# Optimization experiments

Hardware: AMD Instinct MI355X
Metric: run time of the kernel (lower is better)

## Reference

```python
import jax, jax.numpy as jnp
import numpy as np

H = 512

def setup_inputs() -> dict:
    key = jax.random.key(0)
    ks = jax.random.split(key, 8)
    b, s, m, n, h = 8, 128, 32, 64, H
    sc = 1.0 / np.sqrt(h)
    return {
        "x": jax.random.normal(ks[0], (b, s, m, h), dtype=jnp.float32),
        "y": jax.random.normal(ks[1], (b, s, n, h), dtype=jnp.float32),
        # MultiHeadSelfAtt (additive self-attentive pooling: b*m*h -> b*h)
        "Wa1": jax.random.normal(ks[2], (h, h), dtype=jnp.float32) * sc,
        "ba1": jnp.zeros((h,), dtype=jnp.float32),
        "wa2": jax.random.normal(ks[3], (h,), dtype=jnp.float32) * sc,
        # gate Linear(2h -> h), torch layout weight: (h, 2h)
        "Wl": jax.random.normal(ks[4], (h, 2 * h), dtype=jnp.float32) * (1.0 / np.sqrt(2 * h)),
        "bl": jnp.zeros((h,), dtype=jnp.float32),
    }

def reference(x, y, Wa1, ba1, wa2, Wl, bl):
    h = x.shape[-1]
    # attentive pooling over m for every (b, s) slice: b s m h -> b s h
    scores = jnp.tanh(x @ Wa1 + ba1) @ wa2          # b s m
    attn = jax.nn.softmax(scores, axis=-1)
    pooled = jnp.einsum('bsm,bsmh->bsh', attn, x)   # b s h
    # step i (i>=1) uses pooled x at step i-1
    i_x = pooled[:, :-1]                            # b (s-1) h
    Wy, Wi = Wl[:, :h], Wl[:, h:]                   # split concat-linear
    pre = jnp.einsum('bsnh,gh->bsng', y[:, 1:], Wy) \
        + (i_x @ Wi.T + bl)[:, :, None, :]          # b (s-1) n h
    gate = jax.nn.sigmoid(pre)
    out_rest = y[:, 1:] + i_x[:, :, None, :] * gate
    return jnp.concatenate([y[:, :1], out_rest], axis=1)  # b s n h
```

## Files before the change

### kernel.cpp

```cpp
#include <hip/hip_runtime.h>
#include <cstdint>
#include <cstddef>

#define H 512
#define SEQ 128

typedef __bf16 v8bf __attribute__((ext_vector_type(8)));
typedef float v4f __attribute__((ext_vector_type(4)));

__device__ __forceinline__ unsigned short f2bf(float f) {
    unsigned int u = __float_as_uint(f);
    u = (u + 0x7FFFu + ((u >> 16) & 1u)) >> 16;
    return (unsigned short)u;
}
__device__ __forceinline__ float bf2f(unsigned short h) {
    return __uint_as_float(((unsigned int)h) << 16);
}
__device__ __forceinline__ v8bf load_bf8(const unsigned short* p) {
    return *reinterpret_cast<const v8bf*>(p);
}
__device__ __forceinline__ float fast_tanh(float v) {
    float e = __expf(2.f * v);
    return 1.f - 2.f * __builtin_amdgcn_rcpf(e + 1.f);
}
__device__ __forceinline__ float fast_sigmoid(float v) {
    return __builtin_amdgcn_rcpf(1.f + __expf(-v));
}


__global__ __launch_bounds__(256) void prep_kernel(
        const float* __restrict__ Wa1, const float* __restrict__ Wl,
        unsigned short* __restrict__ WyS, unsigned short* __restrict__ WiS,
        unsigned short* __restrict__ WaS) {
    int tg = blockIdx.x * 256 + threadIdx.x;
    int mat = tg >> 15;
    int idx = tg & 32767;
    int lane = idx & 63;
    int ks = (idx >> 6) & 15;
    int c = idx >> 10;
    int g = c * 16 + (lane & 15);
    int hb = ks * 32 + ((lane >> 4) << 3);
    unsigned short o[8];
    unsigned short* dst;
    if (mat == 0) {
        const float* s = Wl + (size_t)g * 1024 + hb;
#pragma unroll
        for (int j = 0; j < 8; ++j) o[j] = f2bf(s[j]);
        dst = WyS + (size_t)idx * 8;
    } else if (mat == 1) {
        const float* s = Wl + (size_t)g * 1024 + 512 + hb;
#pragma unroll
        for (int j = 0; j < 8; ++j) o[j] = f2bf(s[j]);
        dst = WiS + (size_t)idx * 8;
    } else {
#pragma unroll
        for (int j = 0; j < 8; ++j) o[j] = f2bf(Wa1[(size_t)(hb + j) * H + g]);
        dst = WaS + (size_t)idx * 8;
    }
    *reinterpret_cast<ushort4*>(dst)     = *reinterpret_cast<ushort4*>(&o[0]);
    *reinterpret_cast<ushort4*>(dst + 4) = *reinterpret_cast<ushort4*>(&o[4]);
}

__global__ __launch_bounds__(256, 3) void attn_pool_kernel(
        const float* __restrict__ x, const unsigned short* __restrict__ WaS,
        const float* __restrict__ ba1, const float* __restrict__ wa2,
        float* __restrict__ ixf, unsigned short* __restrict__ ixb) {
    __shared__ __align__(16) unsigned short Xb[32][520];
    __shared__ float attn[32];
    __shared__ float scpart[4][32];

    int bid = blockIdx.x;
    int b = bid / 127, s = bid % 127;
    int t = threadIdx.x;

    const float4* x4 = reinterpret_cast<const float4*>(x + (size_t)(b * SEQ + s) * 32 * H);
#pragma unroll
    for (int i = 0; i < 16; ++i) {
        int idx4 = t + i * 256;
        float4 v = x4[idx4];
        int e = idx4 * 4, m = e >> 9, h = e & 511;
        ushort4 o;
        o.x = f2bf(v.x); o.y = f2bf(v.y); o.z = f2bf(v.z); o.w = f2bf(v.w);
        *reinterpret_cast<ushort4*>(&Xb[m][h]) = o;
    }
    __syncthreads();

    int w = t >> 6, lane = t & 63, q = lane >> 4, c16 = lane & 15;

    v4f acc[2][8];
#pragma unroll
    for (int mi = 0; mi < 2; ++mi)
#pragma unroll
        for (int ci = 0; ci < 8; ++ci) acc[mi][ci] = (v4f){0.f, 0.f, 0.f, 0.f};

    const unsigned short* Bb = WaS + (size_t)(w * 8 * 16) * 512 + lane * 8;

#pragma unroll
    for (int ks = 0; ks < 16; ++ks) {
        v8bf a0 = load_bf8(&Xb[c16][ks * 32 + q * 8]);
        v8bf a1 = load_bf8(&Xb[16 + c16][ks * 32 + q * 8]);
#pragma unroll
        for (int ci = 0; ci < 8; ++ci) {
            v8bf bb = load_bf8(Bb + (size_t)(ci * 16 + ks) * 512);
            acc[0][ci] = __builtin_amdgcn_mfma_f32_16x16x32_bf16(a0, bb, acc[0][ci], 0, 0, 0);
            acc[1][ci] = __builtin_amdgcn_mfma_f32_16x16x32_bf16(a1, bb, acc[1][ci], 0, 0, 0);
        }
    }

    float sr[2][4] = {{0.f, 0.f, 0.f, 0.f}, {0.f, 0.f, 0.f, 0.f}};
#pragma unroll
    for (int ci = 0; ci < 8; ++ci) {
        int g = (w * 8 + ci) * 16 + c16;
        float w2 = wa2[g];
        float bv = ba1[g];
#pragma unroll
        for (int mi = 0; mi < 2; ++mi)
#pragma unroll
            for (int i = 0; i < 4; ++i)
                sr[mi][i] += w2 * fast_tanh(acc[mi][ci][i] + bv);
    }
#pragma unroll
    for (int off = 1; off < 16; off <<= 1) {
#pragma unroll
        for (int mi = 0; mi < 2; ++mi)
#pragma unroll
            for (int i = 0; i < 4; ++i) sr[mi][i] += __shfl_xor(sr[mi][i], off);
    }
    if (c16 == 0) {
#pragma unroll
        for (int mi = 0; mi < 2; ++mi)
#pragma unroll
            for (int i = 0; i < 4; ++i) scpart[w][mi * 16 + q * 4 + i] = sr[mi][i];
    }
    __syncthreads();

    if (t == 0) {
        float sc[32];
        float mx = -1e30f;
#pragma unroll
        for (int m = 0; m < 32; ++m) {
            float v = scpart[0][m] + scpart[1][m] + scpart[2][m] + scpart[3][m];
            sc[m] = v;
            mx = fmaxf(mx, v);
        }
        float sum = 0.f;
#pragma unroll
        for (int m = 0; m < 32; ++m) {
            float e = __expf(sc[m] - mx);
            attn[m] = e;
            sum += e;
        }
        float inv = 1.f / sum;
#pragma unroll
        for (int m = 0; m < 32; ++m) attn[m] *= inv;
    }
    __syncthreads();

    int h0 = t * 2;
    float p0 = 0.f, p1 = 0.f;
#pragma unroll
    for (int m = 0; m < 32; ++m) {
        float am = attn[m];
        p0 += am * bf2f(Xb[m][h0]);
        p1 += am * bf2f(Xb[m][h0 + 1]);
    }
    size_t r = (size_t)bid;
    ixf[r * H + h0] = p0;
    ixf[r * H + h0 + 1] = p1;
    ixb[r * H + h0] = f2bf(p0);
    ixb[r * H + h0 + 1] = f2bf(p1);
}

__global__ __launch_bounds__(256) void ipre_kernel(
        const unsigned short* __restrict__ ixb, const unsigned short* __restrict__ WiS,
        const float* __restrict__ bl, float* __restrict__ ipre) {
    int row16 = blockIdx.x * 16;
    int t = threadIdx.x, w = t >> 6, lane = t & 63, q = lane >> 4, c16 = lane & 15;
    int c0 = blockIdx.y * 8 + w * 2;

    v4f acc0 = {0.f, 0.f, 0.f, 0.f};
    v4f acc1 = {0.f, 0.f, 0.f, 0.f};
    const unsigned short* arow = ixb + (size_t)(row16 + c16) * H + q * 8;
#pragma unroll
    for (int ks = 0; ks < 16; ++ks) {
        v8bf a = load_bf8(arow + ks * 32);
        acc0 = __builtin_amdgcn_mfma_f32_16x16x32_bf16(
            a, load_bf8(WiS + (size_t)(c0 * 16 + ks) * 512 + lane * 8), acc0, 0, 0, 0);
        acc1 = __builtin_amdgcn_mfma_f32_16x16x32_bf16(
            a, load_bf8(WiS + (size_t)((c0 + 1) * 16 + ks) * 512 + lane * 8), acc1, 0, 0, 0);
    }
#pragma unroll
    for (int cc = 0; cc < 2; ++cc) {
        int g = (c0 + cc) * 16 + c16;
        float blv = bl[g];
        v4f a = cc ? acc1 : acc0;
#pragma unroll
        for (int i = 0; i < 4; ++i) {
            int row = row16 + q * 4 + i;
            if (row < 1016) ipre[(size_t)row * H + g] = a[i] + blv;
        }
    }
}

__global__ __launch_bounds__(256, 2) void main_kernel(
        const float* __restrict__ y, const unsigned short* __restrict__ WyS,
        const float* __restrict__ ixf, const float* __restrict__ ipre,
        float* __restrict__ out) {
    int s = blockIdx.x, b = blockIdx.y;
    int t = threadIdx.x;
    size_t base = (size_t)(b * SEQ + s) * 64 * H;

    if (s == 0) {
        const float4* y4 = reinterpret_cast<const float4*>(y + base);
        float4* o4 = reinterpret_cast<float4*>(out + base);
#pragma unroll
        for (int i = 0; i < 32; ++i) o4[t + i * 256] = y4[t + i * 256];
        return;
    }

    __shared__ __align__(16) unsigned short Yb[64][520];
    __shared__ float ip_s[512];
    __shared__ float ix_s[512];

    int r = b * 127 + (s - 1);
    const float4* y4 = reinterpret_cast<const float4*>(y + base);
#pragma unroll
    for (int i = 0; i < 32; ++i) {
        int idx4 = t + i * 256;
        float4 v = y4[idx4];
        int e = idx4 * 4, n = e >> 9, h = e & 511;
        ushort4 o;
        o.x = f2bf(v.x); o.y = f2bf(v.y); o.z = f2bf(v.z); o.w = f2bf(v.w);
        *reinterpret_cast<ushort4*>(&Yb[n][h]) = o;
    }
    ip_s[t]       = ipre[(size_t)r * H + t];
    ip_s[t + 256] = ipre[(size_t)r * H + t + 256];
    ix_s[t]       = ixf[(size_t)r * H + t];
    ix_s[t + 256] = ixf[(size_t)r * H + t + 256];
    __syncthreads();

    int w = t >> 6, lane = t & 63, q = lane >> 4, c16 = lane & 15;

#pragma unroll
    for (int pass = 0; pass < 2; ++pass) {
        v4f acc[4][4];
#pragma unroll
        for (int rt = 0; rt < 4; ++rt)
#pragma unroll
            for (int ci = 0; ci < 4; ++ci) acc[rt][ci] = (v4f){0.f, 0.f, 0.f, 0.f};

        const unsigned short* Bb = WyS + (size_t)((w * 8 + pass * 4) * 16) * 512 + lane * 8;

#pragma unroll
        for (int ks = 0; ks < 16; ++ks) {
            v8bf a[4];
#pragma unroll
            for (int rt = 0; rt < 4; ++rt)
                a[rt] = load_bf8(&Yb[rt * 16 + c16][ks * 32 + q * 8]);
#pragma unroll
            for (int ci = 0; ci < 4; ++ci) {
                v8bf bb = load_bf8(Bb + (size_t)(ci * 16 + ks) * 512);
#pragma unroll
                for (int rt = 0; rt < 4; ++rt)
                    acc[rt][ci] = __builtin_amdgcn_mfma_f32_16x16x32_bf16(
                        a[rt], bb, acc[rt][ci], 0, 0, 0);
            }
        }

#pragma unroll
        for (int ci = 0; ci < 4; ++ci) {
            int g = (w * 8 + pass * 4 + ci) * 16 + c16;
            float ip = ip_s[g];
            float ixv = ix_s[g];
#pragma unroll
            for (int rt = 0; rt < 4; ++rt)
#pragma unroll
                for (int i = 0; i < 4; ++i) {
                    int n = rt * 16 + q * 4 + i;
                    float pre = acc[rt][ci][i] + ip;
                    float gate = fast_sigmoid(pre);
                    out[base + (size_t)n * H + g] = bf2f(Yb[n][g]) + ixv * gate;
                }
        }
    }
}

extern "C" void kernel_launch(void* const* d_in, const int* in_sizes, int n_in,
                              void* d_out, int out_size, void* d_ws, size_t ws_size,
                              hipStream_t stream) {
    const float* x   = (const float*)d_in[0];
    const float* y   = (const float*)d_in[1];
    const float* Wa1 = (const float*)d_in[2];
    const float* ba1 = (const float*)d_in[3];
    const float* wa2 = (const float*)d_in[4];
    const float* Wl  = (const float*)d_in[5];
    const float* bl  = (const float*)d_in[6];
    float* out = (float*)d_out;

    char* ws = (char*)d_ws;
    unsigned short* WyS  = (unsigned short*)(ws);
    unsigned short* WiS  = (unsigned short*)(ws + 524288);
    unsigned short* WaS  = (unsigned short*)(ws + 1048576);
    float*          ixf  = (float*)(ws + 1572864);
    unsigned short* ixb  = (unsigned short*)(ws + 3670016);
    float*          ipre = (float*)(ws + 4718592);

    hipLaunchKernelGGL(prep_kernel, dim3(384), dim3(256), 0, stream, Wa1, Wl, WyS, WiS, WaS);
    hipLaunchKernelGGL(attn_pool_kernel, dim3(1016), dim3(256), 0, stream,
                       x, WaS, ba1, wa2, ixf, ixb);
    hipLaunchKernelGGL(ipre_kernel, dim3(64, 4), dim3(256), 0, stream, ixb, WiS, bl, ipre);
    hipLaunchKernelGGL(main_kernel, dim3(128, 8), dim3(256), 0, stream,
                       y, WyS, ixf, ipre, out);
}
```

Baseline: 175.2 us.

## Split main kernel rows across two blocks and parallelize softmax with shuffles

The main gating kernel now assigns half of the 64 n-rows to each block, which doubles the grid, halves LDS use and raises the occupancy hint from 2 to 4 blocks. The inner loop is restructured into a single pass over 2 row tiles by 8 column tiles. Each WyS weight fragment is therefore loaded from global or cache once per pair of row tiles, where it used to be reused across four row tiles. The attention softmax in the pooling kernel is changed from a serial single-thread loop to a warp shuffle reduction. Together these add parallelism and latency hiding, at the cost of more total weight-load traffic.

```diff
diff --git a/kernel.cpp b/kernel.cpp
--- a/kernel.cpp
+++ b/kernel.cpp
@@ -134,25 +134,17 @@
     }
     __syncthreads();
 
-    if (t == 0) {
-        float sc[32];
-        float mx = -1e30f;
-#pragma unroll
-        for (int m = 0; m < 32; ++m) {
-            float v = scpart[0][m] + scpart[1][m] + scpart[2][m] + scpart[3][m];
-            sc[m] = v;
-            mx = fmaxf(mx, v);
-        }
-        float sum = 0.f;
-#pragma unroll
-        for (int m = 0; m < 32; ++m) {
-            float e = __expf(sc[m] - mx);
-            attn[m] = e;
-            sum += e;
-        }
-        float inv = 1.f / sum;
-#pragma unroll
-        for (int m = 0; m < 32; ++m) attn[m] *= inv;
+    if (t < 64) {
+        int m = t & 31;
+        float v = scpart[0][m] + scpart[1][m] + scpart[2][m] + scpart[3][m];
+        float mx = v;
+#pragma unroll
+        for (int off = 1; off < 32; off <<= 1) mx = fmaxf(mx, __shfl_xor(mx, off));
+        float e = __expf(v - mx);
+        float sum = e;
+#pragma unroll
+        for (int off = 1; off < 32; off <<= 1) sum += __shfl_xor(sum, off);
+        if (t < 32) attn[m] = e * __builtin_amdgcn_rcpf(sum);
     }
     __syncthreads();
 
@@ -202,30 +194,33 @@
     }
 }
 
-__global__ __launch_bounds__(256, 2) void main_kernel(
+__global__ __launch_bounds__(256, 4) void main_kernel(
         const float* __restrict__ y, const unsigned short* __restrict__ WyS,
         const float* __restrict__ ixf, const float* __restrict__ ipre,
         float* __restrict__ out) {
-    int s = blockIdx.x, b = blockIdx.y;
+    int half = blockIdx.x & 1;
+    int s = blockIdx.x >> 1;
+    int b = blockIdx.y;
     int t = threadIdx.x;
-    size_t base = (size_t)(b * SEQ + s) * 64 * H;
+    size_t base  = (size_t)(b * SEQ + s) * 64 * H;
+    size_t rbase = base + (size_t)half * 32 * H;
 
     if (s == 0) {
-        const float4* y4 = reinterpret_cast<const float4*>(y + base);
-        float4* o4 = reinterpret_cast<float4*>(out + base);
-#pragma unroll
-        for (int i = 0; i < 32; ++i) o4[t + i * 256] = y4[t + i * 256];
+        const float4* y4 = reinterpret_cast<const float4*>(y + rbase);
+        float4* o4 = reinterpret_cast<float4*>(out + rbase);
+#pragma unroll
+        for (int i = 0; i < 16; ++i) o4[t + i * 256] = y4[t + i * 256];
         return;
     }
 
-    __shared__ __align__(16) unsigned short Yb[64][520];
+    __shared__ __align__(16) unsigned short Yb[32][520];
     __shared__ float ip_s[512];
     __shared__ float ix_s[512];
 
     int r = b * 127 + (s - 1);
-    const float4* y4 = reinterpret_cast<const float4*>(y + base);
-#pragma unroll
-    for (int i = 0; i < 32; ++i) {
+    const float4* y4 = reinterpret_cast<const float4*>(y + rbase);
+#pragma unroll
+    for (int i = 0; i < 16; ++i) {
         int idx4 = t + i * 256;
         float4 v = y4[idx4];
         int e = idx4 * 4, n = e >> 9, h = e & 511;
@@ -241,47 +236,40 @@
 
     int w = t >> 6, lane = t & 63, q = lane >> 4, c16 = lane & 15;
 
-#pragma unroll
-    for (int pass = 0; pass < 2; ++pass) {
-        v4f acc[4][4];
-#pragma unroll
-        for (int rt = 0; rt < 4; ++rt)
-#pragma unroll
-            for (int ci = 0; ci < 4; ++ci) acc[rt][ci] = (v4f){0.f, 0.f, 0.f, 0.f};
-
-        const unsigned short* Bb = WyS + (size_t)((w * 8 + pass * 4) * 16) * 512 + lane * 8;
-
-#pragma unroll
-        for (int ks = 0; ks < 16; ++ks) {
-            v8bf a[4];
-#pragma unroll
-            for (int rt = 0; rt < 4; ++rt)
-                a[rt] = load_bf8(&Yb[rt * 16 + c16][ks * 32 + q * 8]);
-#pragma unroll
-            for (int ci = 0; ci < 4; ++ci) {
-                v8bf bb = load_bf8(Bb + (size_t)(ci * 16 + ks) * 512);
-#pragma unroll
-                for (int rt = 0; rt < 4; ++rt)
-                    acc[rt][ci] = __builtin_amdgcn_mfma_f32_16x16x32_bf16(
-                        a[rt], bb, acc[rt][ci], 0, 0, 0);
+    v4f acc[2][8];
+#pragma unroll
+    for (int rt = 0; rt < 2; ++rt)
+#pragma unroll
+        for (int ci = 0; ci < 8; ++ci) acc[rt][ci] = (v4f){0.f, 0.f, 0.f, 0.f};
+
+    const unsigned short* Bb = WyS + (size_t)(w * 8 * 16) * 512 + lane * 8;
+
+#pragma unroll
+    for (int ks = 0; ks < 16; ++ks) {
+        v8bf a0 = load_bf8(&Yb[c16][ks * 32 + q * 8]);
+        v8bf a1 = load_bf8(&Yb[16 + c16][ks * 32 + q * 8]);
+#pragma unroll
+        for (int ci = 0; ci < 8; ++ci) {
+            v8bf bb = load_bf8(Bb + (size_t)(ci * 16 + ks) * 512);
+            acc[0][ci] = __builtin_amdgcn_mfma_f32_16x16x32_bf16(a0, bb, acc[0][ci], 0, 0, 0);
+            acc[1][ci] = __builtin_amdgcn_mfma_f32_16x16x32_bf16(a1, bb, acc[1][ci], 0, 0, 0);
+        }
+    }
+
+#pragma unroll
+    for (int ci = 0; ci < 8; ++ci) {
+        int g = (w * 8 + ci) * 16 + c16;
+        float ip = ip_s[g];
+        float ixv = ix_s[g];
+#pragma unroll
+        for (int rt = 0; rt < 2; ++rt)
+#pragma unroll
+            for (int i = 0; i < 4; ++i) {
+                int nl = rt * 16 + q * 4 + i;
+                float pre = acc[rt][ci][i] + ip;
+                float gate = fast_sigmoid(pre);
+                out[rbase + (size_t)nl * H + g] = bf2f(Yb[nl][g]) + ixv * gate;
             }
-        }
-
-#pragma unroll
-        for (int ci = 0; ci < 4; ++ci) {
-            int g = (w * 8 + pass * 4 + ci) * 16 + c16;
-            float ip = ip_s[g];
-            float ixv = ix_s[g];
-#pragma unroll
-            for (int rt = 0; rt < 4; ++rt)
-#pragma unroll
-                for (int i = 0; i < 4; ++i) {
-                    int n = rt * 16 + q * 4 + i;
-                    float pre = acc[rt][ci][i] + ip;
-                    float gate = fast_sigmoid(pre);
-                    out[base + (size_t)n * H + g] = bf2f(Yb[n][g]) + ixv * gate;
-                }
-        }
     }
 }
 
@@ -309,6 +297,6 @@
     hipLaunchKernelGGL(attn_pool_kernel, dim3(1016), dim3(256), 0, stream,
                        x, WaS, ba1, wa2, ixf, ixb);
     hipLaunchKernelGGL(ipre_kernel, dim3(64, 4), dim3(256), 0, stream, ixb, WiS, bl, ipre);
-    hipLaunchKernelGGL(main_kernel, dim3(128, 8), dim3(256), 0, stream,
+    hipLaunchKernelGGL(main_kernel, dim3(256, 8), dim3(256), 0, stream,
                        y, WyS, ixf, ipre, out);
 }
```

Result: slower. 194.4 us (+11.0%).

## Pipeline y staging with MFMA over K chunks and parallelize softmax across lanes

Applied to the files above, without the earlier changes.

The gate kernel now loads y in four 128-column K chunks, prefetching the next chunk into registers while the MFMAs run on the current chunk already in LDS. It also merges the two output passes into one with a 4x8 accumulator array, so the A fragments from LDS are reused across all 8 column tiles. This raises register pressure to 128 accumulator floats plus 32 prefetch floats, which may cut occupancy. Separately, the pooling kernel's serial single-thread softmax over 32 scores is replaced by a wavefront-shuffle reduction.

```diff
diff --git a/kernel.cpp b/kernel.cpp
--- a/kernel.cpp
+++ b/kernel.cpp
@@ -134,25 +134,17 @@
     }
     __syncthreads();
 
-    if (t == 0) {
-        float sc[32];
-        float mx = -1e30f;
-#pragma unroll
-        for (int m = 0; m < 32; ++m) {
-            float v = scpart[0][m] + scpart[1][m] + scpart[2][m] + scpart[3][m];
-            sc[m] = v;
-            mx = fmaxf(mx, v);
-        }
-        float sum = 0.f;
-#pragma unroll
-        for (int m = 0; m < 32; ++m) {
-            float e = __expf(sc[m] - mx);
-            attn[m] = e;
-            sum += e;
-        }
-        float inv = 1.f / sum;
-#pragma unroll
-        for (int m = 0; m < 32; ++m) attn[m] *= inv;
+    if (t < 64) {
+        int m = t & 31;
+        float v = scpart[0][m] + scpart[1][m] + scpart[2][m] + scpart[3][m];
+        float mx = v;
+#pragma unroll
+        for (int off = 1; off < 32; off <<= 1) mx = fmaxf(mx, __shfl_xor(mx, off));
+        float e = __expf(v - mx);
+        float sum = e;
+#pragma unroll
+        for (int off = 1; off < 32; off <<= 1) sum += __shfl_xor(sum, off);
+        if (t < 32) attn[m] = e * __builtin_amdgcn_rcpf(sum);
     }
     __syncthreads();
 
@@ -224,64 +216,86 @@
 
     int r = b * 127 + (s - 1);
     const float4* y4 = reinterpret_cast<const float4*>(y + base);
-#pragma unroll
-    for (int i = 0; i < 32; ++i) {
-        int idx4 = t + i * 256;
-        float4 v = y4[idx4];
-        int e = idx4 * 4, n = e >> 9, h = e & 511;
-        ushort4 o;
-        o.x = f2bf(v.x); o.y = f2bf(v.y); o.z = f2bf(v.z); o.w = f2bf(v.w);
-        *reinterpret_cast<ushort4*>(&Yb[n][h]) = o;
+
+    float4 cur[8];
+#pragma unroll
+    for (int jj = 0; jj < 8; ++jj) {
+        int q4 = t + jj * 256;
+        cur[jj] = y4[(q4 >> 5) * 128 + (q4 & 31)];
     }
     ip_s[t]       = ipre[(size_t)r * H + t];
     ip_s[t + 256] = ipre[(size_t)r * H + t + 256];
     ix_s[t]       = ixf[(size_t)r * H + t];
     ix_s[t + 256] = ixf[(size_t)r * H + t + 256];
-    __syncthreads();
 
     int w = t >> 6, lane = t & 63, q = lane >> 4, c16 = lane & 15;
 
-#pragma unroll
-    for (int pass = 0; pass < 2; ++pass) {
-        v4f acc[4][4];
-#pragma unroll
-        for (int rt = 0; rt < 4; ++rt)
-#pragma unroll
-            for (int ci = 0; ci < 4; ++ci) acc[rt][ci] = (v4f){0.f, 0.f, 0.f, 0.f};
-
-        const unsigned short* Bb = WyS + (size_t)((w * 8 + pass * 4) * 16) * 512 + lane * 8;
-
-#pragma unroll
-        for (int ks = 0; ks < 16; ++ks) {
+    v4f acc[4][8];
+#pragma unroll
+    for (int rt = 0; rt < 4; ++rt)
+#pragma unroll
+        for (int ci = 0; ci < 8; ++ci) acc[rt][ci] = (v4f){0.f, 0.f, 0.f, 0.f};
+
+    const unsigned short* Bb = WyS + (size_t)(w * 8 * 16) * 512 + lane * 8;
+
+#pragma unroll
+    for (int c = 0; c < 4; ++c) {
+        float4 nxt[8];
+        if (c < 3) {
+#pragma unroll
+            for (int jj = 0; jj < 8; ++jj) {
+                int q4 = t + jj * 256;
+                nxt[jj] = y4[(q4 >> 5) * 128 + (c + 1) * 32 + (q4 & 31)];
+            }
+        }
+#pragma unroll
+        for (int jj = 0; jj < 8; ++jj) {
+            int q4 = t + jj * 256;
+            int row = q4 >> 5, colf4 = q4 & 31;
+            ushort4 o;
+            o.x = f2bf(cur[jj].x); o.y = f2bf(cur[jj].y);
+            o.z = f2bf(cur[jj].z); o.w = f2bf(cur[jj].w);
+            *reinterpret_cast<ushort4*>(&Yb[row][c * 128 + colf4 * 4]) = o;
+        }
+        asm volatile("s_waitcnt lgkmcnt(0)" ::: "memory");
+        __builtin_amdgcn_s_barrier();
+
+#pragma unroll
+        for (int ks = 0; ks < 4; ++ks) {
+            int ksg = c * 4 + ks;
             v8bf a[4];
 #pragma unroll
             for (int rt = 0; rt < 4; ++rt)
-                a[rt] = load_bf8(&Yb[rt * 16 + c16][ks * 32 + q * 8]);
-#pragma unroll
-            for (int ci = 0; ci < 4; ++ci) {
-                v8bf bb = load_bf8(Bb + (size_t)(ci * 16 + ks) * 512);
+                a[rt] = load_bf8(&Yb[rt * 16 + c16][ksg * 32 + q * 8]);
+#pragma unroll
+            for (int ci = 0; ci < 8; ++ci) {
+                v8bf bb = load_bf8(Bb + (size_t)(ci * 16 + ksg) * 512);
 #pragma unroll
                 for (int rt = 0; rt < 4; ++rt)
                     acc[rt][ci] = __builtin_amdgcn_mfma_f32_16x16x32_bf16(
                         a[rt], bb, acc[rt][ci], 0, 0, 0);
             }
         }
-
-#pragma unroll
-        for (int ci = 0; ci < 4; ++ci) {
-            int g = (w * 8 + pass * 4 + ci) * 16 + c16;
-            float ip = ip_s[g];
-            float ixv = ix_s[g];
-#pragma unroll
-            for (int rt = 0; rt < 4; ++rt)
-#pragma unroll
-                for (int i = 0; i < 4; ++i) {
-                    int n = rt * 16 + q * 4 + i;
-                    float pre = acc[rt][ci][i] + ip;
-                    float gate = fast_sigmoid(pre);
-                    out[base + (size_t)n * H + g] = bf2f(Yb[n][g]) + ixv * gate;
-                }
-        }
+        if (c < 3) {
+#pragma unroll
+            for (int jj = 0; jj < 8; ++jj) cur[jj] = nxt[jj];
+        }
+    }
+
+#pragma unroll
+    for (int ci = 0; ci < 8; ++ci) {
+        int g = (w * 8 + ci) * 16 + c16;
+        float ip = ip_s[g];
+        float ixv = ix_s[g];
+#pragma unroll
+        for (int rt = 0; rt < 4; ++rt)
+#pragma unroll
+            for (int i = 0; i < 4; ++i) {
+                int n = rt * 16 + q * 4 + i;
+                float pre = acc[rt][ci][i] + ip;
+                float gate = fast_sigmoid(pre);
+                out[base + (size_t)n * H + g] = bf2f(Yb[n][g]) + ixv * gate;
+            }
     }
 }
 
```

Result: slower. 200.8 us (+14.6%).
